# Kernel optimization log

Measured on AMD Instinct MI355X. Metric: run time of the kernel, lower is better.

Reference implementation:

```python
import jax, jax.numpy as jnp
import numpy as np

N, E, D = 50000, 800000, 64  # nodes, edges, hidden (in_hid == out_hid, n_heads == 1)


def setup_inputs() -> dict:
    key = jax.random.key(0)
    ks = jax.random.split(key, 12)

    def lin(k, out_d, in_d):
        k1, k2 = jax.random.split(k)
        s = 1.0 / np.sqrt(in_d)
        W = jax.random.uniform(k1, (out_d, in_d), minval=-s, maxval=s, dtype=jnp.float32)
        b = jax.random.uniform(k2, (out_d,), minval=-s, maxval=s, dtype=jnp.float32)
        return W, b

    Wt, bt = lin(ks[0], D, D + 1)   # w_transfer: Linear(d_input+1, d_k)
    Wq, bq = lin(ks[1], D, D)
    Wks, bks = lin(ks[2], D, D)
    Wkd, bkd = lin(ks[3], D, D)
    Wvs, bvs = lin(ks[4], D, D)
    Wvd, bvd = lin(ks[5], D, D)
    return {
        "x": jax.random.normal(ks[6], (N, D), dtype=jnp.float32),
        "edge_index": jax.random.randint(ks[7], (2, E), 0, N),
        "edge_time": jax.random.uniform(ks[8], (E,), dtype=jnp.float32),
        "x_time": jax.random.uniform(ks[9], (N,), dtype=jnp.float32),
        "edge_same": jax.random.randint(ks[10], (E,), 0, 2).astype(jnp.float32),
        "ln_gamma": jnp.ones((D,), jnp.float32),
        "ln_beta": jnp.zeros((D,), jnp.float32),
        "Wt": Wt, "bt": bt, "Wq": Wq, "bq": bq,
        "Wks": Wks, "bks": bks, "Wkd": Wkd, "bkd": bkd,
        "Wvs": Wvs, "bvs": bvs, "Wvd": Wvd, "bvd": bvd,
    }


def _gelu(x):
    return jax.nn.gelu(x, approximate=False)  # torch F.gelu default (erf)


def _temporal_enc(t):
    # TemporalEncoding: div_term[j] = 1/10000^(2*(j//2)/D); sin on even cols, cos on odd
    j = jnp.arange(D)
    div = 1.0 / jnp.power(jnp.float32(10000.0), (2.0 * (j // 2)).astype(jnp.float32) / D)
    pe = (t.reshape(-1, 1) * 200.0) * div[None, :]  # [E, D]
    return jnp.where((j % 2 == 0)[None, :], jnp.sin(pe), jnp.cos(pe))


def reference(x, edge_index, edge_time, x_time, edge_same, ln_gamma, ln_beta,
              Wt, bt, Wq, bq, Wks, bks, Wkd, bkd, Wvs, bvs, Wvd, bvd):
    residual = x
    # LayerNorm(d_input)
    mu = jnp.mean(x, axis=-1, keepdims=True)
    var = jnp.var(x, axis=-1, keepdims=True)
    xn = (x - mu) / jnp.sqrt(var + 1e-5) * ln_gamma + ln_beta

    src, dst = edge_index[0], edge_index[1]  # x_j = source, x_i = target (PyG default)
    x_j = xn[src]                            # [E, D] gather
    x_i = xn[dst]                            # [E, D] gather
    es = edge_same.reshape(-1, 1)            # [E, 1]

    te = _temporal_enc(edge_time)            # [E, D]
    xt = _gelu(jnp.concatenate([x_j, edge_time.reshape(-1, 1)], axis=1) @ Wt.T + bt) + te

    q = x_i @ Wq.T + bq
    k = es * (xt @ Wks.T + bks) + (1.0 - es) * (xt @ Wkd.T + bkd)
    att = jnp.sum(k * q, axis=-1) / jnp.sqrt(jnp.float32(D))  # [E]

    # PyG-style segment softmax over edges sharing the same receiver
    m = jax.ops.segment_max(att, dst, num_segments=N)
    m = jnp.where(jnp.isfinite(m), m, 0.0)
    ex = jnp.exp(att - m[dst])
    denom = jax.ops.segment_sum(ex, dst, num_segments=N)
    attn = ex / (denom[dst] + 1e-16)         # [E]

    v = es * (xt @ Wvs.T + bvs) + (1.0 - es) * (xt @ Wvd.T + bvd)
    aggr = jax.ops.segment_sum(attn[:, None] * v, dst, num_segments=N)  # [N, D]

    return residual + _gelu(aggr)            # dropout is identity in eval
```

## Files before the change

kernel.cpp:

```cpp
#include <hip/hip_runtime.h>
#include <hip/hip_bf16.h>
#include <math.h>

#define D 64

typedef __attribute__((ext_vector_type(8))) short bf16x8;
typedef __attribute__((ext_vector_type(8))) _Float16 f16x8;
typedef __attribute__((ext_vector_type(8))) unsigned short u16x8;
typedef __attribute__((ext_vector_type(4))) float f32x4;
typedef unsigned short u16;

__device__ __forceinline__ float gelu_erf(float x) {
    return 0.5f * x * (1.0f + erff(x * 0.70710678118654752f));
}
__device__ __forceinline__ float gelu_fast(float x) {
    float t = x * fmaf(x * x, -0.1029432f, -2.3022080f);
    float e = __builtin_amdgcn_exp2f(t);
    return x * __builtin_amdgcn_rcpf(1.0f + e);
}
__device__ __forceinline__ u16 f2bf(float v) {
    __hip_bfloat16 h = __float2bfloat16(v);
    return *(u16*)&h;
}
__device__ __forceinline__ float bf2f(u16 v) {
    return __uint_as_float(((unsigned int)v) << 16);
}
__device__ __forceinline__ u16 f2h(float v) {
    _Float16 h = (_Float16)v;
    return __builtin_bit_cast(u16, h);
}
__device__ __forceinline__ unsigned pk2h(float lo, float hi) {
    return (unsigned)f2h(lo) | ((unsigned)f2h(hi) << 16);
}
__device__ __forceinline__ void atomic_pk_add_u32(u16* addr, unsigned p) {
    asm volatile("global_atomic_pk_add_f16 %0, %1, off sc1" :: "v"(addr), "v"(p));
}
__device__ __forceinline__ void atomic_pk_add_f16(u16* addr, float lo, float hi) {
    atomic_pk_add_u32(addr, pk2h(lo, hi));
}
__device__ __forceinline__ int pi_perm(int p) { return ((p & 3) << 4) | (p >> 2); }

__device__ __forceinline__ float rowsum16(float v) {
    int x;
    x = __builtin_amdgcn_update_dpp(0, __builtin_bit_cast(int, v), 0xB1, 0xF, 0xF, true);
    v += __builtin_bit_cast(float, x);
    x = __builtin_amdgcn_update_dpp(0, __builtin_bit_cast(int, v), 0x4E, 0xF, 0xF, true);
    v += __builtin_bit_cast(float, x);
    x = __builtin_amdgcn_update_dpp(0, __builtin_bit_cast(int, v), 0x141, 0xF, 0xF, true);
    v += __builtin_bit_cast(float, x);
    x = __builtin_amdgcn_update_dpp(0, __builtin_bit_cast(int, v), 0x140, 0xF, 0xF, true);
    v += __builtin_bit_cast(float, x);
    return v;
}

__global__ __launch_bounds__(256) void prep_hist(
    const float* __restrict__ Wt, const float* __restrict__ Wq,
    const float* __restrict__ Wks, const float* __restrict__ Wkd,
    const float* __restrict__ Wvs, const float* __restrict__ Wvd,
    u16* __restrict__ WtB, u16* __restrict__ WqB,
    u16* __restrict__ WksB, u16* __restrict__ WkdB,
    u16* __restrict__ WvsB, u16* __restrict__ WvdB,
    const int* __restrict__ ei, const float* __restrict__ esame,
    int* __restrict__ cnt, int* __restrict__ rank, int E)
{
    if (blockIdx.x < 12) {
        int task = blockIdx.x * 4 + (threadIdx.x >> 6);
        int lane = threadIdx.x & 63;
        int wsel = task >> 3, f = task & 7;
        int c = lane & 15, quad = lane >> 4;
        int nt = f >> 1, kk = f & 1;
        for (int j = 0; j < 8; ++j) {
            int n = nt * 16 + c, k = kk * 32 + quad * 8 + j;
            float v; u16* dp; bool h16 = false;
            switch (wsel) {
                case 0: v = Wt[n * 65 + k];  dp = WtB;  break;
                case 1: v = Wq[n * 64 + k];  dp = WqB;  break;
                case 2: v = Wks[k * 64 + n]; dp = WksB; break;
                case 3: v = Wkd[k * 64 + n]; dp = WkdB; break;
                case 4: v = Wvs[n * 64 + pi_perm(k)]; dp = WvsB; h16 = true; break;
                default: v = Wvd[n * 64 + pi_perm(k)]; dp = WvdB; h16 = true; break;
            }
            dp[(f * 64 + lane) * 8 + j] = h16 ? f2h(v) : f2bf(v);
        }
    } else {
        int gid = (blockIdx.x - 12) * 256 + threadIdx.x;
        int stride = (gridDim.x - 12) * 256;
        int e[4]; bool v[4]; int key[4];
        #pragma unroll
        for (int j = 0; j < 4; ++j) { e[j] = gid + j * stride; v[j] = e[j] < E; }
        #pragma unroll
        for (int j = 0; j < 4; ++j) {
            if (v[j]) key[j] = 2 * ei[E + e[j]] + (esame[e[j]] > 0.5f ? 0 : 1);
        }
        int r[4];
        #pragma unroll
        for (int j = 0; j < 4; ++j) {
            if (v[j]) r[j] = atomicAdd(&cnt[key[j]], 1);
        }
        #pragma unroll
        for (int j = 0; j < 4; ++j) {
            if (v[j]) rank[e[j]] = r[j];
        }
    }
}

#define SCAN_CHUNK 2048

__global__ __launch_bounds__(256) void scan_phaseA(const int* __restrict__ cnt,
                                                   int* __restrict__ bsum, int M)
{
    int base = blockIdx.x * SCAN_CHUNK;
    int s = 0;
    for (int i = threadIdx.x; i < SCAN_CHUNK; i += 256) {
        int idx = base + i;
        s += (idx < M) ? cnt[idx] : 0;
    }
    #pragma unroll
    for (int o = 32; o; o >>= 1) s += __shfl_xor(s, o);
    __shared__ int red[4];
    if ((threadIdx.x & 63) == 0) red[threadIdx.x >> 6] = s;
    __syncthreads();
    if (threadIdx.x == 0) bsum[blockIdx.x] = red[0] + red[1] + red[2] + red[3];
}

__global__ __launch_bounds__(256) void scan_phaseC(const int* __restrict__ cnt,
                                                   const int* __restrict__ bsum,
                                                   int* __restrict__ cursor, int M)
{
    __shared__ int wsum[4];
    __shared__ int sboff;
    if (threadIdx.x < 64) {
        int v = ((int)threadIdx.x < (int)blockIdx.x) ? bsum[threadIdx.x] : 0;
        #pragma unroll
        for (int o = 32; o; o >>= 1) v += __shfl_xor(v, o);
        if (threadIdx.x == 0) sboff = v;
    }
    int base = blockIdx.x * SCAN_CHUNK;
    int i0 = base + threadIdx.x * 8;
    int vals[8];
    int tsum = 0;
    #pragma unroll
    for (int j = 0; j < 8; ++j) {
        int idx = i0 + j;
        vals[j] = (idx < M) ? cnt[idx] : 0;
        tsum += vals[j];
    }
    int lane = threadIdx.x & 63;
    int w = threadIdx.x >> 6;
    int inc = tsum;
    #pragma unroll
    for (int o = 1; o < 64; o <<= 1) {
        int v = __shfl_up(inc, o);
        if (lane >= o) inc += v;
    }
    if (lane == 63) wsum[w] = inc;
    __syncthreads();
    int woff = 0;
    #pragma unroll
    for (int k = 0; k < 4; ++k) woff += (k < w) ? wsum[k] : 0;
    int excl = woff + (inc - tsum) + sboff;
    #pragma unroll
    for (int j = 0; j < 8; ++j) {
        int idx = i0 + j;
        if (idx < M) cursor[idx] = excl;
        excl += vals[j];
    }
}

__global__ __launch_bounds__(256) void scatter_qgemm(
    const int* __restrict__ ei, const float* __restrict__ et,
    const float* __restrict__ esame, const int* __restrict__ cursor,
    const int* __restrict__ rank,
    int4* __restrict__ evk, int E, int GS,
    const float* __restrict__ x, const float* __restrict__ gamma, const float* __restrict__ beta,
    const u16* __restrict__ WqB, const u16* __restrict__ WksB, const u16* __restrict__ WkdB,
    const float* __restrict__ bq, const float* __restrict__ bks, const float* __restrict__ bkd,
    u16* __restrict__ xnb, u16* __restrict__ qk2, float* __restrict__ bq2, int N)
{
    __shared__ u16 qtile[4][16 * 64];
    __shared__ u16 stile[4][32 * 64];

    if (blockIdx.x < GS) {
        int gid = blockIdx.x * 256 + threadIdx.x;
        int stride = GS * 256;
        int e[4]; bool v[4]; int key[4]; int rk[4]; int src[4]; float tv[4];
        #pragma unroll
        for (int j = 0; j < 4; ++j) { e[j] = gid + j * stride; v[j] = e[j] < E; }
        #pragma unroll
        for (int j = 0; j < 4; ++j) {
            if (v[j]) {
                key[j] = 2 * ei[E + e[j]] + (esame[e[j]] > 0.5f ? 0 : 1);
                rk[j] = rank[e[j]];
                src[j] = ei[e[j]];
                tv[j] = et[e[j]];
            }
        }
        int pos[4];
        #pragma unroll
        for (int j = 0; j < 4; ++j) {
            if (v[j]) pos[j] = cursor[key[j]] + rk[j];
        }
        #pragma unroll
        for (int j = 0; j < 4; ++j) {
            if (v[j]) evk[pos[j]] = make_int4(key[j], __float_as_int(tv[j]), src[j], 0);
        }
        return;
    }

    const int lane = threadIdx.x & 63;
    const int c = lane & 15, quad = lane >> 4;
    const int w = threadIdx.x >> 6;
    const int wave = (blockIdx.x - GS) * 4 + w;
    const int n0r = wave * 16;
    const bool active = n0r < N;
    const int n0 = active ? n0r : 0;
    const int rowA = (n0 + c < N) ? n0 + c : N - 1;

    const float* xrow = x + (long)rowA * D;
    f32x4 xa = *(const f32x4*)(xrow + quad * 8);
    f32x4 xb = *(const f32x4*)(xrow + quad * 8 + 4);
    f32x4 xc = *(const f32x4*)(xrow + 32 + quad * 8);
    f32x4 xd = *(const f32x4*)(xrow + 32 + quad * 8 + 4);
    float s = 0.f, s2 = 0.f;
    #pragma unroll
    for (int j = 0; j < 4; ++j) {
        s += xa[j] + xb[j] + xc[j] + xd[j];
        s2 += xa[j] * xa[j] + xb[j] * xb[j] + xc[j] * xc[j] + xd[j] * xd[j];
    }
    s += __shfl_xor(s, 16);  s += __shfl_xor(s, 32);
    s2 += __shfl_xor(s2, 16); s2 += __shfl_xor(s2, 32);
    float mu = s * (1.0f / 64.0f);
    float var = s2 * (1.0f / 64.0f) - mu * mu;
    float rinv = rsqrtf(var + 1e-5f);
    f32x4 ga = *(const f32x4*)(gamma + quad * 8);
    f32x4 gb = *(const f32x4*)(gamma + quad * 8 + 4);
    f32x4 gc = *(const f32x4*)(gamma + 32 + quad * 8);
    f32x4 gd = *(const f32x4*)(gamma + 32 + quad * 8 + 4);
    f32x4 ba = *(const f32x4*)(beta + quad * 8);
    f32x4 bb = *(const f32x4*)(beta + quad * 8 + 4);
    f32x4 bc = *(const f32x4*)(beta + 32 + quad * 8);
    f32x4 bd = *(const f32x4*)(beta + 32 + quad * 8 + 4);
    bf16x8 a0, a1;
    #pragma unroll
    for (int j = 0; j < 4; ++j) {
        a0[j]     = (short)f2bf(fmaf((xa[j] - mu) * rinv, ga[j], ba[j]));
        a0[4 + j] = (short)f2bf(fmaf((xb[j] - mu) * rinv, gb[j], bb[j]));
        a1[j]     = (short)f2bf(fmaf((xc[j] - mu) * rinv, gc[j], bc[j]));
        a1[4 + j] = (short)f2bf(fmaf((xd[j] - mu) * rinv, gd[j], bd[j]));
    }
    *(bf16x8*)(xnb + (long)rowA * D + quad * 8) = a0;
    *(bf16x8*)(xnb + (long)rowA * D + 32 + quad * 8) = a1;

    float bqc[4], bksc[4], bkdc[4];
    #pragma unroll
    for (int t = 0; t < 4; ++t) {
        bqc[t] = bq[t * 16 + c]; bksc[t] = bks[t * 16 + c]; bkdc[t] = bkd[t * 16 + c];
    }

    f32x4 accq[4];
    #pragma unroll
    for (int t = 0; t < 4; ++t) {
        bf16x8 b0 = *(const bf16x8*)(WqB + ((t * 2 + 0) * 64 + lane) * 8);
        bf16x8 b1 = *(const bf16x8*)(WqB + ((t * 2 + 1) * 64 + lane) * 8);
        f32x4 z = {0.f, 0.f, 0.f, 0.f};
        z = __builtin_amdgcn_mfma_f32_16x16x32_bf16(a0, b0, z, 0, 0, 0);
        z = __builtin_amdgcn_mfma_f32_16x16x32_bf16(a1, b1, z, 0, 0, 0);
        accq[t] = z;
    }
    #pragma unroll
    for (int r = 0; r < 4; ++r) {
        float qv[4], ss = 0.f, sd = 0.f;
        #pragma unroll
        for (int t = 0; t < 4; ++t) {
            qv[t] = accq[t][r] + bqc[t];
            ss = fmaf(qv[t], bksc[t], ss);
            sd = fmaf(qv[t], bkdc[t], sd);
        }
        #pragma unroll
        for (int o = 1; o < 16; o <<= 1) { ss += __shfl_xor(ss, o); sd += __shfl_xor(sd, o); }
        int nrow = n0 + quad * 4 + r;
        if (active && c == 0 && nrow < N)
            *(float2*)(bq2 + 2 * nrow) = make_float2(ss, sd);
        #pragma unroll
        for (int t = 0; t < 4; ++t)
            qtile[w][(quad * 4 + r) * 64 + t * 16 + c] = f2bf(qv[t]);
    }
    __syncthreads();

    const u16* qrow = &qtile[w][c * 64 + quad * 8];
    bf16x8 q0 = *(const bf16x8*)(qrow);
    bf16x8 q1 = *(const bf16x8*)(qrow + 32);
    #pragma unroll
    for (int t = 0; t < 4; ++t) {
        bf16x8 bs0 = *(const bf16x8*)(WksB + ((t * 2 + 0) * 64 + lane) * 8);
        bf16x8 bs1 = *(const bf16x8*)(WksB + ((t * 2 + 1) * 64 + lane) * 8);
        bf16x8 bd0 = *(const bf16x8*)(WkdB + ((t * 2 + 0) * 64 + lane) * 8);
        bf16x8 bd1 = *(const bf16x8*)(WkdB + ((t * 2 + 1) * 64 + lane) * 8);
        f32x4 zs = {0.f, 0.f, 0.f, 0.f}, zd = {0.f, 0.f, 0.f, 0.f};
        zs = __builtin_amdgcn_mfma_f32_16x16x32_bf16(q0, bs0, zs, 0, 0, 0);
        zs = __builtin_amdgcn_mfma_f32_16x16x32_bf16(q1, bs1, zs, 0, 0, 0);
        zd = __builtin_amdgcn_mfma_f32_16x16x32_bf16(q0, bd0, zd, 0, 0, 0);
        zd = __builtin_amdgcn_mfma_f32_16x16x32_bf16(q1, bd1, zd, 0, 0, 0);
        #pragma unroll
        for (int r = 0; r < 4; ++r) {
            int m = quad * 4 + r;
            stile[w][(2 * m + 0) * 64 + c * 4 + t] = f2bf(zs[r]);
            stile[w][(2 * m + 1) * 64 + c * 4 + t] = f2bf(zd[r]);
        }
    }
    __syncthreads();
    if (active) {
        int nrows = min(16, N - n0);
        const u16x8* sp = (const u16x8*)&stile[w][0];
        u16x8* dp = (u16x8*)(qk2 + (long)(2 * n0) * D);
        int cnt8 = nrows * 16;
        for (int j = lane; j < cnt8; j += 64) dp[j] = sp[j];
    }
}

template<bool FULL>
__device__ __forceinline__ void edge_run(
    const int4* __restrict__ evk, const u16* __restrict__ xnb,
    const u16* wfrag, const float* btc, const float* w64c,
    const float* dvr, float phr,
    const u16* __restrict__ qk2, const float* __restrict__ bq2,
    u16* __restrict__ A, float* __restrict__ den,
    int base, int end, int qchunk, int c, int quad)
{
    const float S = 0.18033688011f;
    const int lane = quad * 16 + c;
    int cur_key = -1;
    float racc0 = 0.f, racc1 = 0.f, racc2 = 0.f, racc3 = 0.f, rden = 0.f;
    ushort4 q4 = {0, 0, 0, 0};
    float bqv = 0.f;
    int stash_key = -1; unsigned sp01 = 0, sp23 = 0; float srden = 0.f;

    const int rowbase = base + (c >> 2) * qchunk + (c & 3);
    const int qbase   = base + quad * qchunk;
    const int last    = end - 1;

    int srcC = ((const int*)(evk + (FULL ? rowbase : min(rowbase, last))))[2];

    for (int i = 0; i < qchunk; i += 4) {
        const u16* ar = xnb + srcC * D + quad * 8;
        bf16x8 a0 = *(const bf16x8*)(ar);
        bf16x8 a1 = *(const bf16x8*)(ar + 32);

        srcC = ((const int*)(evk + min(rowbase + i + 4, last)))[2];

        int qb = qbase + i;
        int2 kt0 = *(const int2*)(evk + (FULL ? qb     : min(qb,     last)));
        int2 kt1 = *(const int2*)(evk + (FULL ? qb + 1 : min(qb + 1, last)));
        int2 kt2 = *(const int2*)(evk + (FULL ? qb + 2 : min(qb + 2, last)));
        int2 kt3 = *(const int2*)(evk + (FULL ? qb + 3 : min(qb + 3, last)));

        if (stash_key >= 0) {
            u16* ap = A + stash_key * D + c * 4;
            atomic_pk_add_u32(ap, sp01);
            atomic_pk_add_u32(ap + 2, sp23);
            if (c == 0) atomicAdd(&den[stash_key], srden);
            stash_key = -1;
        }

        unsigned woff = 0;
        asm volatile("" : "+v"(woff));
        const u16* wfx = wfrag + woff;

        f32x4 acc[4];
        #pragma unroll
        for (int t = 0; t < 4; ++t) {
            bf16x8 b0 = *(const bf16x8*)(wfx + ((t * 2 + 0) * 64 + lane) * 8);
            bf16x8 b1 = *(const bf16x8*)(wfx + ((t * 2 + 1) * 64 + lane) * 8);
            f32x4 z = {btc[t], btc[t], btc[t], btc[t]};
            z = __builtin_amdgcn_mfma_f32_16x16x32_bf16(a0, b0, z, 0, 0, 0);
            z = __builtin_amdgcn_mfma_f32_16x16x32_bf16(a1, b1, z, 0, 0, 0);
            acc[t] = z;
        }

        #pragma unroll
        for (int r = 0; r < 4; ++r) {
            int2 kt = (r == 0) ? kt0 : (r == 1) ? kt1 : (r == 2) ? kt2 : kt3;
            int keym = kt.x;
            float tm = __int_as_float(kt.y);

            float x0 = fmaf(tm, w64c[0], acc[0][r]);
            float x1 = fmaf(tm, w64c[1], acc[1][r]);
            float x2 = fmaf(tm, w64c[2], acc[2][r]);
            float x3 = fmaf(tm, w64c[3], acc[3][r]);
            float v0 = gelu_fast(x0) + __builtin_amdgcn_sinf(fmaf(tm, dvr[0], phr));
            float v1 = gelu_fast(x1) + __builtin_amdgcn_sinf(fmaf(tm, dvr[1], phr));
            float v2 = gelu_fast(x2) + __builtin_amdgcn_sinf(fmaf(tm, dvr[2], phr));
            float v3 = gelu_fast(x3) + __builtin_amdgcn_sinf(fmaf(tm, dvr[3], phr));

            if (keym != cur_key) {
                ushort4 nq = *(const ushort4*)(qk2 + keym * D + c * 4);
                float nb = bq2[keym];
                if (cur_key >= 0) {
                    if (stash_key >= 0) {
                        u16* ap = A + stash_key * D + c * 4;
                        atomic_pk_add_u32(ap, sp01);
                        atomic_pk_add_u32(ap + 2, sp23);
                        if (c == 0) atomicAdd(&den[stash_key], srden);
                    }
                    sp01 = pk2h(racc0, racc1);
                    sp23 = pk2h(racc2, racc3);
                    srden = rden;
                    stash_key = cur_key;
                }
                cur_key = keym;
                q4 = nq;
                bqv = nb * S;
                racc0 = racc1 = racc2 = racc3 = 0.f;
                rden = 0.f;
            }

            float p = v0 * bf2f(q4.x);
            p = fmaf(v1, bf2f(q4.y), p);
            p = fmaf(v2, bf2f(q4.z), p);
            p = fmaf(v3, bf2f(q4.w), p);
            p = rowsum16(p);

            float ex = __builtin_amdgcn_exp2f(fmaf(p, S, bqv));
            if (!FULL && (qbase + i + r >= end)) ex = 0.f;

            racc0 = fmaf(ex, v0, racc0);
            racc1 = fmaf(ex, v1, racc1);
            racc2 = fmaf(ex, v2, racc2);
            racc3 = fmaf(ex, v3, racc3);
            rden += ex;
        }
    }

    if (stash_key >= 0) {
        u16* ap = A + stash_key * D + c * 4;
        atomic_pk_add_u32(ap, sp01);
        atomic_pk_add_u32(ap + 2, sp23);
        if (c == 0) atomicAdd(&den[stash_key], srden);
    }
    if (cur_key >= 0) {
        u16* ap = A + cur_key * D + c * 4;
        atomic_pk_add_f16(ap, racc0, racc1);
        atomic_pk_add_f16(ap + 2, racc2, racc3);
        if (c == 0) atomicAdd(&den[cur_key], rden);
    }
}

__global__ __launch_bounds__(256) void edge_pass(
    const int4* __restrict__ evk, const u16* __restrict__ xnb, const u16* __restrict__ WtB,
    const float* __restrict__ Wt, const float* __restrict__ bt,
    const u16* __restrict__ qk2, const float* __restrict__ bq2,
    u16* __restrict__ A, float* __restrict__ den, int E, int chunk)
{
    __shared__ u16 wfrag[4096];
    {
        u16x8* wf = (u16x8*)wfrag;
        const u16x8* ws = (const u16x8*)WtB;
        wf[threadIdx.x] = ws[threadIdx.x];
        wf[threadIdx.x + 256] = ws[threadIdx.x + 256];
    }
    __syncthreads();

    const int lane = threadIdx.x & 63;
    const int c = lane & 15, quad = lane >> 4;
    const int wave = blockIdx.x * 4 + (threadIdx.x >> 6);
    const int base = wave * chunk;
    if (base >= E) return;
    const int end = min(base + chunk, E);
    const int qchunk = chunk >> 2;

    float btc[4], w64c[4], dvr[4];
    #pragma unroll
    for (int t = 0; t < 4; ++t) {
        int dim = t * 16 + c;
        btc[t] = bt[dim];
        w64c[t] = Wt[dim * 65 + 64];
        dvr[t] = 31.830988618f * expf(-9.210340371976184f * (float)(2 * (dim >> 1)) * (1.0f / 64.0f));
    }
    const float phr = (c & 1) ? 0.25f : 0.0f;

    if (base + chunk <= E)
        edge_run<true>(evk, xnb, wfrag, btc, w64c, dvr, phr, qk2, bq2, A, den,
                       base, end, qchunk, c, quad);
    else
        edge_run<false>(evk, xnb, wfrag, btc, w64c, dvr, phr, qk2, bq2, A, den,
                        base, end, qchunk, c, quad);
}

__global__ __launch_bounds__(256) void vgemm(
    const float* __restrict__ x, const u16* __restrict__ A, const float* __restrict__ den,
    const u16* __restrict__ WvsB, const u16* __restrict__ WvdB,
    const float* __restrict__ bvs, const float* __restrict__ bvd,
    float* __restrict__ out, int N)
{
    const int lane = threadIdx.x & 63;
    const int c = lane & 15, quad = lane >> 4;
    const int wave = blockIdx.x * 4 + (threadIdx.x >> 6);
    const int n0 = wave * 16;
    if (n0 >= N) return;
    const int rowA = (n0 + c < N) ? n0 + c : N - 1;

    float bvsc[4], bvdc[4];
    #pragma unroll
    for (int t = 0; t < 4; ++t) { bvsc[t] = bvs[t * 16 + c]; bvdc[t] = bvd[t * 16 + c]; }

    const u16* srow = A + (long)(2 * rowA) * D + quad * 8;
    const u16* drow = A + (long)(2 * rowA + 1) * D + quad * 8;
    f16x8 s0 = *(const f16x8*)(srow);
    f16x8 s1 = *(const f16x8*)(srow + 32);
    f16x8 d0 = *(const f16x8*)(drow);
    f16x8 d1 = *(const f16x8*)(drow + 32);

    f32x4 oacc[4];
    #pragma unroll
    for (int t = 0; t < 4; ++t) {
        f16x8 bs0 = *(const f16x8*)(WvsB + ((t * 2 + 0) * 64 + lane) * 8);
        f16x8 bs1 = *(const f16x8*)(WvsB + ((t * 2 + 1) * 64 + lane) * 8);
        f16x8 bd0 = *(const f16x8*)(WvdB + ((t * 2 + 0) * 64 + lane) * 8);
        f16x8 bd1 = *(const f16x8*)(WvdB + ((t * 2 + 1) * 64 + lane) * 8);
        f32x4 z = {0.f, 0.f, 0.f, 0.f};
        z = __builtin_amdgcn_mfma_f32_16x16x32_f16(s0, bs0, z, 0, 0, 0);
        z = __builtin_amdgcn_mfma_f32_16x16x32_f16(s1, bs1, z, 0, 0, 0);
        z = __builtin_amdgcn_mfma_f32_16x16x32_f16(d0, bd0, z, 0, 0, 0);
        z = __builtin_amdgcn_mfma_f32_16x16x32_f16(d1, bd1, z, 0, 0, 0);
        oacc[t] = z;
    }

    #pragma unroll
    for (int r = 0; r < 4; ++r) {
        int n = n0 + quad * 4 + r;
        if (n >= N) continue;
        float ds = den[2 * n], dd = den[2 * n + 1];
        float inv = 1.0f / (ds + dd + 1e-16f);
        float fs = ds * inv, fd = dd * inv;
        #pragma unroll
        for (int t = 0; t < 4; ++t) {
            long idx = (long)n * D + t * 16 + c;
            float o = fmaf(oacc[t][r], inv, fmaf(fs, bvsc[t], fd * bvdc[t]));
            out[idx] = x[idx] + gelu_erf(o);
        }
    }
}

extern "C" void kernel_launch(void* const* d_in, const int* in_sizes, int n_in,
                              void* d_out, int out_size, void* d_ws, size_t ws_size,
                              hipStream_t stream) {
    const float* x        = (const float*)d_in[0];
    const int*   ei       = (const int*)d_in[1];
    const float* et       = (const float*)d_in[2];
    const float* esame    = (const float*)d_in[4];
    const float* ln_gamma = (const float*)d_in[5];
    const float* ln_beta  = (const float*)d_in[6];
    const float* Wt  = (const float*)d_in[7];
    const float* bt  = (const float*)d_in[8];
    const float* Wq  = (const float*)d_in[9];
    const float* bq  = (const float*)d_in[10];
    const float* Wks = (const float*)d_in[11];
    const float* bks = (const float*)d_in[12];
    const float* Wkd = (const float*)d_in[13];
    const float* bkd = (const float*)d_in[14];
    const float* Wvs = (const float*)d_in[15];
    const float* bvs = (const float*)d_in[16];
    const float* Wvd = (const float*)d_in[17];
    const float* bvd = (const float*)d_in[18];
    float* out = (float*)d_out;

    const int N = in_sizes[0] / D;
    const int E = in_sizes[2];
    const int M = 2 * N;

    u16* A      = (u16*)d_ws;
    float* den  = (float*)(A + (long)M * D);
    int* cnt    = (int*)(den + M);
    int* cursor = cnt + M;
    float* bq2  = (float*)(cursor + M);
    int4* evk   = (int4*)(bq2 + M);
    int* bsum   = (int*)(evk + E);
    u16* xnb    = (u16*)(bsum + 256);
    u16* qk2    = xnb + (long)N * D;
    u16* WtB    = qk2 + (long)M * D;
    u16* WqB    = WtB + 4096;
    u16* WksB   = WqB + 4096;
    u16* WkdB   = WksB + 4096;
    u16* WvsB   = WkdB + 4096;
    u16* WvdB   = WvsB + 4096;

    char* wsend = (char*)(WvdB + 4096);
    const size_t usedBytes = (size_t)(wsend - (char*)d_ws);
    const size_t rankBytes = (size_t)E * 4;
    const bool rank_standalone = (ws_size >= usedBytes + rankBytes);
    int* rank = rank_standalone ? (int*)wsend : (int*)A;

    if (rank_standalone) {
        hipMemsetAsync(A, 0, (size_t)M * D * 2 + (size_t)M * 4 * 2, stream);
    } else {
        hipMemsetAsync((char*)A + rankBytes, 0,
                       ((size_t)M * D * 2 - rankBytes) + (size_t)M * 4 * 2, stream);
    }

    const int GH = (E + 256 * 4 - 1) / (256 * 4);
    prep_hist<<<12 + GH, 256, 0, stream>>>(Wt, Wq, Wks, Wkd, Wvs, Wvd,
                                           WtB, WqB, WksB, WkdB, WvsB, WvdB,
                                           ei, esame, cnt, rank, E);
    const int nbScan = (M + SCAN_CHUNK - 1) / SCAN_CHUNK;
    scan_phaseA<<<nbScan, 256, 0, stream>>>(cnt, bsum, M);
    scan_phaseC<<<nbScan, 256, 0, stream>>>(cnt, bsum, cursor, M);

    const int GS = (E + 256 * 4 - 1) / (256 * 4);
    const int GQ = ((N + 15) / 16 + 3) / 4;
    scatter_qgemm<<<GS + GQ, 256, 0, stream>>>(
        ei, et, esame, cursor, rank, evk, E, GS,
        x, ln_gamma, ln_beta, WqB, WksB, WkdB, bq, bks, bkd,
        xnb, qk2, bq2, N);

    if (!rank_standalone)
        hipMemsetAsync(A, 0, rankBytes, stream);

    const int nwaves = 2048 * 4;
    const int chunk = ((E + nwaves * 16 - 1) / (nwaves * 16)) * 16;
    edge_pass<<<2048, 256, 0, stream>>>(evk, xnb, WtB, Wt, bt,
                                        qk2, bq2, A, den, E, chunk);
    vgemm<<<GQ, 256, 0, stream>>>(x, A, den, WvsB, WvdB, bvs, bvd, out, N);
}
```

Before: 229.1 us.

## Merge two-pass scan into single-block scan and fold accumulator zeroing into qgemm

Replaces the two-kernel chunked prefix scan with one 1024-thread single-block scan over the 100k-entry count array, removing a kernel launch. It also moves the zeroing of the aggregation buffer and denominators from a memset into the Q-GEMM blocks of scatter_qgemm, leaving only the small count memset on the stream. The single-block scan serialises about 100 elements per thread on one CU. The zeroing adds roughly 13 MB of writes to the qgemm blocks.

```diff
diff --git a/kernel.cpp b/kernel.cpp
--- a/kernel.cpp
+++ b/kernel.cpp
@@ -104,66 +104,69 @@
     }
 }
 
-#define SCAN_CHUNK 2048
-
-__global__ __launch_bounds__(256) void scan_phaseA(const int* __restrict__ cnt,
-                                                   int* __restrict__ bsum, int M)
-{
-    int base = blockIdx.x * SCAN_CHUNK;
-    int s = 0;
-    for (int i = threadIdx.x; i < SCAN_CHUNK; i += 256) {
-        int idx = base + i;
-        s += (idx < M) ? cnt[idx] : 0;
-    }
-    #pragma unroll
-    for (int o = 32; o; o >>= 1) s += __shfl_xor(s, o);
-    __shared__ int red[4];
-    if ((threadIdx.x & 63) == 0) red[threadIdx.x >> 6] = s;
-    __syncthreads();
-    if (threadIdx.x == 0) bsum[blockIdx.x] = red[0] + red[1] + red[2] + red[3];
-}
-
-__global__ __launch_bounds__(256) void scan_phaseC(const int* __restrict__ cnt,
-                                                   const int* __restrict__ bsum,
+#define SCAN_T 1024
+__global__ __launch_bounds__(SCAN_T) void scan_one(const int* __restrict__ cnt,
                                                    int* __restrict__ cursor, int M)
 {
-    __shared__ int wsum[4];
-    __shared__ int sboff;
-    if (threadIdx.x < 64) {
-        int v = ((int)threadIdx.x < (int)blockIdx.x) ? bsum[threadIdx.x] : 0;
-        #pragma unroll
-        for (int o = 32; o; o >>= 1) v += __shfl_xor(v, o);
-        if (threadIdx.x == 0) sboff = v;
-    }
-    int base = blockIdx.x * SCAN_CHUNK;
-    int i0 = base + threadIdx.x * 8;
-    int vals[8];
-    int tsum = 0;
-    #pragma unroll
-    for (int j = 0; j < 8; ++j) {
-        int idx = i0 + j;
-        vals[j] = (idx < M) ? cnt[idx] : 0;
-        tsum += vals[j];
-    }
-    int lane = threadIdx.x & 63;
-    int w = threadIdx.x >> 6;
-    int inc = tsum;
+    const int V = (((M + SCAN_T - 1) / SCAN_T) + 3) & ~3;
+    const int t = threadIdx.x;
+    const int beg = t * V;
+
+    int s = 0;
+    for (int j = 0; j < V; j += 4) {
+        int idx = beg + j;
+        if (idx + 3 < M) {
+            int4 v = *(const int4*)(cnt + idx);
+            s += v.x + v.y + v.z + v.w;
+        } else {
+            #pragma unroll
+            for (int k = 0; k < 4; ++k) if (idx + k < M) s += cnt[idx + k];
+        }
+    }
+
+    const int lane = t & 63, w = t >> 6;
+    int inc = s;
     #pragma unroll
     for (int o = 1; o < 64; o <<= 1) {
         int v = __shfl_up(inc, o);
         if (lane >= o) inc += v;
     }
+    __shared__ int wsum[16];
+    __shared__ int woff[16];
     if (lane == 63) wsum[w] = inc;
     __syncthreads();
-    int woff = 0;
-    #pragma unroll
-    for (int k = 0; k < 4; ++k) woff += (k < w) ? wsum[k] : 0;
-    int excl = woff + (inc - tsum) + sboff;
-    #pragma unroll
-    for (int j = 0; j < 8; ++j) {
-        int idx = i0 + j;
-        if (idx < M) cursor[idx] = excl;
-        excl += vals[j];
+    if (w == 0) {
+        int v = (lane < 16) ? wsum[lane] : 0;
+        int a = v;
+        #pragma unroll
+        for (int o = 1; o < 16; o <<= 1) {
+            int u = __shfl_up(a, o);
+            if (lane >= o) a += u;
+        }
+        if (lane < 16) woff[lane] = a - v;
+    }
+    __syncthreads();
+    int excl = woff[w] + (inc - s);
+
+    for (int j = 0; j < V; j += 4) {
+        int idx = beg + j;
+        bool full = (idx + 3 < M);
+        int4 v = {0, 0, 0, 0};
+        if (full) v = *(const int4*)(cnt + idx);
+        else {
+            #pragma unroll
+            for (int k = 0; k < 4; ++k) ((int*)&v)[k] = (idx + k < M) ? cnt[idx + k] : 0;
+        }
+        int4 o;
+        o.x = excl; excl += v.x;
+        o.y = excl; excl += v.y;
+        o.z = excl; excl += v.z;
+        o.w = excl; excl += v.w;
+        if (full) *(int4*)(cursor + idx) = o;
+        else {
+            #pragma unroll
+            for (int k = 0; k < 4; ++k) if (idx + k < M) cursor[idx + k] = ((int*)&o)[k];
+        }
     }
 }
 
@@ -175,7 +178,8 @@
     const float* __restrict__ x, const float* __restrict__ gamma, const float* __restrict__ beta,
     const u16* __restrict__ WqB, const u16* __restrict__ WksB, const u16* __restrict__ WkdB,
     const float* __restrict__ bq, const float* __restrict__ bks, const float* __restrict__ bkd,
-    u16* __restrict__ xnb, u16* __restrict__ qk2, float* __restrict__ bq2, int N)
+    u16* __restrict__ xnb, u16* __restrict__ qk2, float* __restrict__ bq2, int N,
+    int4* __restrict__ zeroDst, long zeroN16)
 {
     __shared__ u16 qtile[4][16 * 64];
     __shared__ u16 stile[4][32 * 64];
@@ -205,6 +209,13 @@
             if (v[j]) evk[pos[j]] = make_int4(key[j], __float_as_int(tv[j]), src[j], 0);
         }
         return;
+    }
+
+    if (zeroDst) {
+        const int nq = (int)gridDim.x - GS;
+        for (long j = (long)(blockIdx.x - GS) * 256 + threadIdx.x; j < zeroN16;
+             j += (long)nq * 256)
+            zeroDst[j] = make_int4(0, 0, 0, 0);
     }
 
     const int lane = threadIdx.x & 63;
@@ -590,27 +601,29 @@
     const bool rank_standalone = (ws_size >= usedBytes + rankBytes);
     int* rank = rank_standalone ? (int*)wsend : (int*)A;
 
+    const size_t adBytes = (size_t)M * D * 2 + (size_t)M * 4;
+
     if (rank_standalone) {
-        hipMemsetAsync(A, 0, (size_t)M * D * 2 + (size_t)M * 4 * 2, stream);
+        hipMemsetAsync(cnt, 0, (size_t)M * 4, stream);
     } else {
         hipMemsetAsync((char*)A + rankBytes, 0,
-                       ((size_t)M * D * 2 - rankBytes) + (size_t)M * 4 * 2, stream);
+                       (adBytes - rankBytes) + (size_t)M * 4, stream);
     }
 
     const int GH = (E + 256 * 4 - 1) / (256 * 4);
     prep_hist<<<12 + GH, 256, 0, stream>>>(Wt, Wq, Wks, Wkd, Wvs, Wvd,
                                            WtB, WqB, WksB, WkdB, WvsB, WvdB,
                                            ei, esame, cnt, rank, E);
-    const int nbScan = (M + SCAN_CHUNK - 1) / SCAN_CHUNK;
-    scan_phaseA<<<nbScan, 256, 0, stream>>>(cnt, bsum, M);
-    scan_phaseC<<<nbScan, 256, 0, stream>>>(cnt, bsum, cursor, M);
+
+    scan_one<<<1, SCAN_T, 0, stream>>>(cnt, cursor, M);
 
     const int GS = (E + 256 * 4 - 1) / (256 * 4);
     const int GQ = ((N + 15) / 16 + 3) / 4;
     scatter_qgemm<<<GS + GQ, 256, 0, stream>>>(
         ei, et, esame, cursor, rank, evk, E, GS,
         x, ln_gamma, ln_beta, WqB, WksB, WkdB, bq, bks, bkd,
-        xnb, qk2, bq2, N);
+        xnb, qk2, bq2, N,
+        rank_standalone ? (int4*)A : (int4*)nullptr, (long)(adBytes / 16));
 
     if (!rank_standalone)
         hipMemsetAsync(A, 0, rankBytes, stream);
```

Measured after the change: 274.6 us. 19.9% more time.
